# Kernel tuning notes

Hardware: AMD Instinct MI355X
Metric: run time of the kernel (lower is better)

The kernel has to match this reference:

```python
import jax, jax.numpy as jnp
import numpy as np

K = 20  # hard-coded k in both DynamicEdgeConv layers


def knn_idx(x, k):
    # pairwise squared distances: |xi|^2 + |xj|^2 - 2 xi.xj  -> [N, N]
    sq = jnp.sum(x * x, axis=-1)
    d = sq[:, None] + sq[None, :] - 2.0 * (x @ x.T)
    _, idx = jax.lax.top_k(-d, k)  # k nearest (self included at dist 0)
    return idx  # [N, k]


def edge_conv(x, idx, W, b):
    # message = MLP([x_i, x_j - x_i]), aggregate = max over neighbors
    xi = x[:, None, :]                       # [N, 1, d]
    xj = x[idx]                              # [N, k, d] gather
    e = jnp.concatenate([jnp.broadcast_to(xi, xj.shape), xj - xi], axis=-1)  # [N, k, 2d]
    h = jax.nn.relu(e @ W + b)               # [N, k, out]
    return jnp.max(h, axis=1)                # [N, out]


def setup_inputs() -> dict:
    key = jax.random.key(0)
    ks = jax.random.split(key, 9)
    N, num_classes = 16384, 40
    s = lambda fan_in: 1.0 / np.sqrt(fan_in)
    return {
        "x": jax.random.normal(ks[0], (N, 3), dtype=jnp.float32),
        "W1": jax.random.normal(ks[1], (6, 64), dtype=jnp.float32) * s(6),
        "b1": jax.random.normal(ks[2], (64,), dtype=jnp.float32) * s(6),
        "W2": jax.random.normal(ks[3], (128, 128), dtype=jnp.float32) * s(128),
        "b2": jax.random.normal(ks[4], (128,), dtype=jnp.float32) * s(128),
        "fc1_w": jax.random.normal(ks[5], (128, 128), dtype=jnp.float32) * s(128),
        "fc1_b": jax.random.normal(ks[6], (128,), dtype=jnp.float32) * s(128),
        "fc2_w": jax.random.normal(ks[7], (128, num_classes), dtype=jnp.float32) * s(128),
        "fc2_b": jax.random.normal(ks[8], (num_classes,), dtype=jnp.float32) * s(128),
    }


def reference(x, W1, b1, W2, b2, fc1_w, fc1_b, fc2_w, fc2_b):
    h = edge_conv(x, knn_idx(x, K), W1, b1)   # [N, 64], kNN on xyz
    h = edge_conv(h, knn_idx(h, K), W2, b2)   # [N, 128], kNN rebuilt on features
    h = jax.nn.relu(h @ fc1_w + fc1_b)
    return h @ fc2_w + fc2_b                  # [N, num_classes]
```

## Files before the change

kernel.cpp:

```cpp
#include <hip/hip_runtime.h>
#include <math.h>

#define N_PTS 16384
#define KNN 20
#define NRANGE 4
#define C_RANGE (N_PTS / NRANGE)
#define QCAPW 256
#define QSW 257
#define HQS 65

#define HBIN_SHIFT 22
#define HBIN_BASE 222

__device__ __forceinline__ unsigned short f2bf(float f) {
  unsigned int u = __float_as_uint(f);
  unsigned int r = (u + 0x7fffu + ((u >> 16) & 1u)) >> 16;
  return (unsigned short)r;
}
__device__ __forceinline__ float bf2f(unsigned short b) {
  return __uint_as_float(((unsigned int)b) << 16);
}

__global__ void pack_kernel(const float* __restrict__ x, float4* __restrict__ xp,
                            unsigned short* __restrict__ xpa,
                            unsigned short* __restrict__ xpb) {
  int i = blockIdx.x*256 + threadIdx.x;
  float v0 = x[i*3+0], v1 = x[i*3+1], v2 = x[i*3+2];
  {
    #pragma clang fp contract(off)
    xp[i] = make_float4(v0, v1, v2, v0*v0 + v1*v1 + v2*v2);
  }
  unsigned int h0 = f2bf(v0), h1 = f2bf(v1), h2 = f2bf(v2);
  unsigned int l0 = f2bf(v0 - bf2f((unsigned short)h0));
  unsigned int l1 = f2bf(v1 - bf2f((unsigned short)h1));
  unsigned int l2 = f2bf(v2 - bf2f((unsigned short)h2));
  unsigned int ua0 = h0 | (h1<<16), ua1 = h2 | (l0<<16), ua2 = l1 | (l2<<16);
  unsigned int ub0 = h0 | (h1<<16), ub1 = h2 | (h0<<16), ub2 = h1 | (h2<<16);
  unsigned int ub3 = l0 | (l1<<16), ub4 = l2 | (l0<<16), ub5 = l1 | (l2<<16);
  uint4* pa = (uint4*)(xpa + (size_t)i*32);
  uint4* pb = (uint4*)(xpb + (size_t)i*32);
  uint4 z; z.x = 0u; z.y = 0u; z.z = 0u; z.w = 0u;
  uint4 A0; A0.x = ua0; A0.y = ua1; A0.z = ua2; A0.w = ua0;
  uint4 A1; A1.x = ua1; A1.y = ua2; A1.z = 0u;  A1.w = 0u;
  uint4 B0; B0.x = ub0; B0.y = ub1; B0.z = ub2; B0.w = ub3;
  uint4 B1; B1.x = ub4; B1.y = ub5; B1.z = 0u;  B1.w = 0u;
  pa[0] = A0; pa[1] = A1; pa[2] = z; pa[3] = z;
  pb[0] = B0; pb[1] = B1; pb[2] = z; pb[3] = z;
}

__global__ void sq64_kernel(const float* __restrict__ h, float* __restrict__ sq) {
  int i = blockIdx.x * blockDim.x + threadIdx.x;
  const float4* r = (const float4*)(h + (long)i*64);
  {
    #pragma clang fp contract(off)
    float ax=0.f, ay=0.f, az=0.f, aw=0.f;
    for (int t=0; t<16; t++) {
      float4 v = r[t];
      ax += v.x*v.x; ay += v.y*v.y; az += v.z*v.z; aw += v.w*v.w;
    }
    sq[i] = (ax+ay)+(az+aw);
  }
}

__global__ void tobf16_kernel(const float* __restrict__ h,
                              unsigned short* __restrict__ bh) {
  int g = blockIdx.x*256 + threadIdx.x;
  float4 v = ((const float4*)h)[g];
  ushort4 hv;
  hv.x = f2bf(v.x); hv.y = f2bf(v.y); hv.z = f2bf(v.z); hv.w = f2bf(v.w);
  ((ushort4*)bh)[g] = hv;
}

__global__ __launch_bounds__(256, 2) void seed64_kernel(const float* __restrict__ h,
                                                        const float* __restrict__ sq,
                                                        const int* __restrict__ idx1,
                                                        float* __restrict__ wsd) {
  int i = blockIdx.x*256 + threadIdx.x;
  float4 q4[16];
  const float4* qrow = (const float4*)(h + (size_t)i*64);
  #pragma unroll
  for (int t=0;t<16;t++) q4[t] = qrow[t];
  float sqi = sq[i];
  float wmax = 0.f;
  for (int k=0;k<KNN;k++) {
    int j = idx1[i*KNN+k];
    const float4* crow = (const float4*)(h + (size_t)j*64);
    float acc = 0.f;
    #pragma unroll 4
    for (int t=0;t<16;t++) {
      float4 c = crow[t];
      acc += q4[t].x*c.x; acc += q4[t].y*c.y; acc += q4[t].z*c.z; acc += q4[t].w*c.w;
    }
    float sqj = sq[j];
    float d = (sqi + sqj) - 2.0f*acc;
    d += (sqi + sqj)*3e-5f + 1e-25f;
    wmax = fmaxf(wmax, d);
  }
  wsd[i] = wmax;
}

__device__ __forceinline__ void t20_replace_rescan(float (&rd)[KNN], int (&ri)[KNN],
                                                   float &maxd, int &maxi, int &maxp,
                                                   float e, int ei) {
  #pragma unroll
  for (int k = 0; k < KNN; k++) if (k == maxp) { rd[k] = e; ri[k] = ei; }
  float md = rd[0]; int mi = ri[0]; int mp = 0;
  #pragma unroll
  for (int k = 1; k < KNN; k++) {
    bool g = (rd[k] > md) || (rd[k] == md && ri[k] > mi);
    md = g ? rd[k] : md; mi = g ? ri[k] : mi; mp = g ? k : mp;
  }
  maxd = md; maxi = mi; maxp = mp;
}

#define WAVE_LDS_FENCE() asm volatile("s_waitcnt lgkmcnt(0)" ::: "memory")

typedef __bf16 bf16x8 __attribute__((ext_vector_type(8)));
typedef float f32x4 __attribute__((ext_vector_type(4)));
#define MFMA16(A,B,C) __builtin_amdgcn_mfma_f32_16x16x32_bf16((A),(B),(C),0,0,0)
#define SCALE3 0.9998f
#define SCALE_HH 0.995f

__device__ __forceinline__ int hbin(float uu) {
  uu = fmaxf(uu, 1e-20f);
  int b = (int)(__float_as_uint(uu) >> HBIN_SHIFT) - HBIN_BASE;
  return b < 0 ? 0 : (b > 63 ? 63 : b);
}

__global__ __launch_bounds__(128, 2) void knn64_wq(const float* __restrict__ h1,
                                                   const unsigned short* __restrict__ hbh,
                                                   const float* __restrict__ sqh,
                                                   const float* __restrict__ wsd,
                                                   float* __restrict__ pd,
                                                   int* __restrict__ pi) {
  __shared__ unsigned short qq[2][32][QSW];
  __shared__ float w19[2][32];
  __shared__ int   cnt[2][32];

  int tid = threadIdx.x;
  int wv = tid >> 6;
  int l  = tid & 63;
  int qb = blockIdx.x >> 2, rg = blockIdx.x & 3;
  int q0 = qb*64, c0 = rg*C_RANGE;
  int qw0 = q0 + wv*32;

  float rd[KNN]; int ri[KNN];
  #pragma unroll
  for (int k = 0; k < KNN; k++) { rd[k] = INFINITY; ri[k] = 0x7fffffff; }
  float maxd = INFINITY; int maxi = 0x7fffffff; int maxp = 0;

  float wsv = INFINITY, sqi = 0.f;
  if (l < 32) {
    wsv = wsd[qw0 + l]; sqi = sqh[qw0 + l];
    w19[wv][l] = wsv; cnt[wv][l] = 0;
  }

  int cn   = l & 15;
  int koff = (l >> 4) * 8;

  bf16x8 a00, a01, a10, a11;
  {
    size_t ar = (size_t)(qw0 + cn) * 64 + koff;
    a00 = *(const bf16x8*)(hbh + ar);
    a01 = *(const bf16x8*)(hbh + ar + 32);
    size_t br = (size_t)(qw0 + 16 + cn) * 64 + koff;
    a10 = *(const bf16x8*)(hbh + br);
    a11 = *(const bf16x8*)(hbh + br + 32);
  }

  float qsl[8], wq[8];
  #pragma unroll
  for (int v = 0; v < 8; v++)
    qsl[v] = sqh[qw0 + (v>>2)*16 + (l>>4)*4 + (v&3)] * SCALE_HH;
  WAVE_LDS_FENCE();
  #pragma unroll
  for (int v = 0; v < 8; v++) wq[v] = w19[wv][(v>>2)*16 + (l>>4)*4 + (v&3)];

  bf16x8 Bp[8], Bq[8]; float Cp[4], Cq[4];

  #define LOADC64(WIN, T0, B, C) do { int cw_ = c0 + (WIN)*256;            \
    _Pragma("unroll")                                                      \
    for (int t_ = 0; t_ < 4; t_++) {                                       \
      size_t br_ = (size_t)(cw_ + ((T0)+t_)*16 + cn) * 64 + koff;          \
      B[2*t_]   = *(const bf16x8*)(hbh + br_);                             \
      B[2*t_+1] = *(const bf16x8*)(hbh + br_ + 32);                        \
      C[t_] = sqh[cw_ + ((T0)+t_)*16 + cn];                                \
    } } while (0)

  #define TILE64(T, B0, B1, CS) do {                                       \
    f32x4 z_ = {0.f, 0.f, 0.f, 0.f};                                       \
    f32x4 d0_ = MFMA16(a00, B0, z_); d0_ = MFMA16(a01, B1, d0_);           \
    f32x4 d1_ = MFMA16(a10, B0, z_); d1_ = MFMA16(a11, B1, d1_);           \
    float csl_ = (CS) * SCALE_HH;                                          \
    _Pragma("unroll")                                                      \
    for (int v = 0; v < 8; v++) {                                          \
      float av_ = (v < 4) ? d0_[v] : d1_[v-4];                             \
      float dd_ = fmaf(-2.f, av_, qsl[v] + csl_);                          \
      if (dd_ <= wq[v]) {                                                  \
        int lq_ = (v>>2)*16 + (l>>4)*4 + (v&3);                            \
        int slot_ = atomicAdd(&cnt[wv][lq_], 1);                           \
        qq[wv][lq_][slot_] = (unsigned short)((T)*16 + cn);                \
      }                                                                    \
    } } while (0)

  #define CHUNK64(B, C, T0)                                                \
    TILE64((T0)+0, B[0], B[1], C[0]); TILE64((T0)+1, B[2], B[3], C[1]);    \
    TILE64((T0)+2, B[4], B[5], C[2]); TILE64((T0)+3, B[6], B[7], C[3])

  LOADC64(0, 0, Bp, Cp);
  for (int win = 0; win < C_RANGE/256; win++) {
    int cw0 = c0 + win*256;
    LOADC64(win, 4, Bq, Cq);
    CHUNK64(Bp, Cp, 0);
    LOADC64(win, 8, Bp, Cp);
    CHUNK64(Bq, Cq, 4);
    LOADC64(win, 12, Bq, Cq);
    CHUNK64(Bp, Cp, 8);
    if (win < C_RANGE/256 - 1) LOADC64(win+1, 0, Bp, Cp);
    CHUNK64(Bq, Cq, 12);

    WAVE_LDS_FENCE();
    int myc = (l < 32) ? cnt[wv][l] : 0;
    if (__any(myc != 0)) {
      if (myc) {
        const float4* qr = (const float4*)(h1 + (size_t)(qw0 + l)*64);
        for (int s = 0; s < myc; s++) {
          int j = cw0 + (int)qq[wv][l][s];
          const float4* cr = (const float4*)(h1 + (size_t)j*64);
          float a = 0.f;
          #pragma unroll 4
          for (int t = 0; t < 16; t++) {
            float4 q = qr[t], c = cr[t];
            a = fmaf(q.x, c.x, a); a = fmaf(q.y, c.y, a);
            a = fmaf(q.z, c.z, a); a = fmaf(q.w, c.w, a);
          }
          float e = (sqi + sqh[j]) - 2.0f*a;
          if (e < maxd || (e == maxd && j < maxi))
            t20_replace_rescan(rd, ri, maxd, maxi, maxp, e, j);
        }
        cnt[wv][l] = 0;
        w19[wv][l] = fminf(maxd, wsv);
      }
      WAVE_LDS_FENCE();
      #pragma unroll
      for (int v = 0; v < 8; v++) wq[v] = w19[wv][(v>>2)*16 + (l>>4)*4 + (v&3)];
    }
  }
  #undef LOADC64
  #undef TILE64
  #undef CHUNK64

  if (l < 32) {
    size_t o = ((size_t)(qw0 + l)*NRANGE + rg)*KNN;
    for (int k = 0; k < KNN; k++) {
      float md = rd[0]; int mi = ri[0]; int mp = 0;
      #pragma unroll
      for (int t = 1; t < KNN; t++) {
        bool g = (rd[t] < md) || (rd[t] == md && ri[t] < mi);
        md = g ? rd[t] : md; mi = g ? ri[t] : mi; mp = g ? t : mp;
      }
      pd[o+k] = md; pi[o+k] = mi;
      #pragma unroll
      for (int t = 0; t < KNN; t++) if (t == mp) rd[t] = INFINITY;
    }
  }
}

__global__ __launch_bounds__(128, 2) void knn3_wq(const float4* __restrict__ xp,
                                                  const unsigned short* __restrict__ xpa,
                                                  const unsigned short* __restrict__ xpb,
                                                  float* __restrict__ pd,
                                                  int* __restrict__ pi) {
  __shared__ unsigned short qq[2][32][QSW];
  __shared__ float w19[2][32];
  __shared__ int   cnt[2][32];

  int tid = threadIdx.x;
  int wv = tid >> 6;
  int l  = tid & 63;
  int qb = blockIdx.x >> 2, rg = blockIdx.x & 3;
  int q0 = qb*64, c0 = rg*C_RANGE;
  int qw0 = q0 + wv*32;

  float rd[KNN]; int ri[KNN];
  #pragma unroll
  for (int k = 0; k < KNN; k++) { rd[k] = INFINITY; ri[k] = 0x7fffffff; }
  float maxd = INFINITY; int maxi = 0x7fffffff; int maxp = 0;

  float4 qv4 = make_float4(0.f, 0.f, 0.f, 0.f);
  if (l < 32) {
    cnt[wv][l] = 0;
    qv4 = xp[qw0 + l];
  }

  int cn   = l & 15;
  int koff = (l >> 4) * 8;

  bf16x8 aq0 = *(const bf16x8*)(xpa + (size_t)(qw0 + cn)*32 + koff);
  bf16x8 aq1 = *(const bf16x8*)(xpa + (size_t)(qw0 + 16 + cn)*32 + koff);

  float qsr[8], qsp[8];
  #pragma unroll
  for (int v = 0; v < 8; v++) {
    qsr[v] = xp[qw0 + (v>>2)*16 + (l>>4)*4 + (v&3)].w;
    qsp[v] = qsr[v] * SCALE3;
  }

  unsigned int* hw = (unsigned int*)&qq[wv][0][0];
  for (int t = l; t < 32*HQS; t += 64) hw[t] = 0u;
  WAVE_LDS_FENCE();

  for (int win = 0; win < 16; win += 4) {
    int cw0 = c0 + win*256;
    #pragma unroll
    for (int t = 0; t < 16; t++) {
      int ct = cw0 + t*16;
      bf16x8 bb = *(const bf16x8*)(xpb + (size_t)(ct + cn)*32 + koff);
      f32x4 z = {0.f, 0.f, 0.f, 0.f};
      f32x4 d0 = MFMA16(aq0, bb, z);
      f32x4 d1 = MFMA16(aq1, bb, z);
      float csr = xp[ct + cn].w;
      #pragma unroll
      for (int v = 0; v < 8; v++) {
        float av = (v < 4) ? d0[v] : d1[v-4];
        float uu = fmaf(-2.f, av, (qsr[v] + csr) * 1.0002f);
        int lq = (v>>2)*16 + (l>>4)*4 + (v&3);
        atomicAdd(&hw[lq*HQS + hbin(uu)], 1u);
      }
    }
  }
  WAVE_LDS_FENCE();

  float wsv = INFINITY;
  if (l < 32) {
    unsigned int c = 0; int bsel = 64;
    for (int b = 0; b < 64; b++) {
      c += hw[l*HQS + b];
      if (bsel == 64 && c >= 20u) bsel = b;
    }
    if (bsel < 63)
      wsv = __uint_as_float((unsigned int)(bsel + HBIN_BASE + 1) << HBIN_SHIFT);
  }
  WAVE_LDS_FENCE();
  if (l < 32) {
    w19[wv][l] = wsv;
    cnt[wv][l] = 0;
  }
  WAVE_LDS_FENCE();
  float wq[8];
  #pragma unroll
  for (int v = 0; v < 8; v++) wq[v] = w19[wv][(v>>2)*16 + (l>>4)*4 + (v&3)];

  bf16x8 Bp[4], Bq[4]; float Cp[4], Cq[4];

  #define LOADC3(WIN, T0, B, C) do { int cw_ = c0 + (WIN)*256;             \
    _Pragma("unroll")                                                      \
    for (int t_ = 0; t_ < 4; t_++) {                                       \
      int ct_ = cw_ + ((T0)+t_)*16;                                        \
      B[t_] = *(const bf16x8*)(xpb + (size_t)(ct_ + cn)*32 + koff);        \
      C[t_] = xp[ct_ + cn].w;                                              \
    } } while (0)

  #define TILE3(T, BB, CS) do {                                            \
    f32x4 z_ = {0.f, 0.f, 0.f, 0.f};                                       \
    f32x4 d0_ = MFMA16(aq0, BB, z_);                                       \
    f32x4 d1_ = MFMA16(aq1, BB, z_);                                       \
    float csp_ = (CS) * SCALE3;                                            \
    _Pragma("unroll")                                                      \
    for (int v = 0; v < 8; v++) {                                          \
      float av_ = (v < 4) ? d0_[v] : d1_[v-4];                             \
      float dd_ = fmaf(-2.f, av_, qsp[v] + csp_);                          \
      if (dd_ <= wq[v]) {                                                  \
        int lq_ = (v>>2)*16 + (l>>4)*4 + (v&3);                            \
        int slot_ = atomicAdd(&cnt[wv][lq_], 1);                           \
        qq[wv][lq_][slot_] = (unsigned short)((T)*16 + cn);                \
      }                                                                    \
    } } while (0)

  #define CHUNK3(B, C, T0)                                                 \
    TILE3((T0)+0, B[0], C[0]); TILE3((T0)+1, B[1], C[1]);                  \
    TILE3((T0)+2, B[2], C[2]); TILE3((T0)+3, B[3], C[3])

  LOADC3(0, 0, Bp, Cp);
  for (int win = 0; win < 16; win++) {
    int cw0 = c0 + win*256;
    LOADC3(win, 4, Bq, Cq);
    CHUNK3(Bp, Cp, 0);
    LOADC3(win, 8, Bp, Cp);
    CHUNK3(Bq, Cq, 4);
    LOADC3(win, 12, Bq, Cq);
    CHUNK3(Bp, Cp, 8);
    if (win < 15) LOADC3(win+1, 0, Bp, Cp);
    CHUNK3(Bq, Cq, 12);

    WAVE_LDS_FENCE();
    int myc = (l < 32) ? cnt[wv][l] : 0;
    if (__any(myc != 0)) {
      if (myc) {
        for (int s = 0; s < myc; s++) {
          int j = cw0 + (int)qq[wv][l][s];
          float4 cv4 = xp[j];
          float e = (qv4.w + cv4.w)
                  - 2.0f*(qv4.x*cv4.x + qv4.y*cv4.y + qv4.z*cv4.z);
          if (e < maxd || (e == maxd && j < maxi))
            t20_replace_rescan(rd, ri, maxd, maxi, maxp, e, j);
        }
        cnt[wv][l] = 0;
        w19[wv][l] = fminf(maxd, wsv);
      }
      WAVE_LDS_FENCE();
      #pragma unroll
      for (int v = 0; v < 8; v++) wq[v] = w19[wv][(v>>2)*16 + (l>>4)*4 + (v&3)];
    }
  }
  #undef LOADC3
  #undef TILE3
  #undef CHUNK3

  if (l < 32) {
    size_t o = ((size_t)(qw0 + l)*NRANGE + rg)*KNN;
    for (int k = 0; k < KNN; k++) {
      float md = rd[0]; int mi = ri[0]; int mp = 0;
      #pragma unroll
      for (int t = 1; t < KNN; t++) {
        bool g = (rd[t] < md) || (rd[t] == md && ri[t] < mi);
        md = g ? rd[t] : md; mi = g ? ri[t] : mi; mp = g ? t : mp;
      }
      pd[o+k] = md; pi[o+k] = mi;
      #pragma unroll
      for (int t = 0; t < KNN; t++) if (t == mp) rd[t] = INFINITY;
    }
  }
}

__global__ void knn_merge_kernel(const float* __restrict__ pd, const int* __restrict__ pi,
                                 int* __restrict__ out_idx) {
  int qi = blockIdx.x*256 + threadIdx.x;
  const float* bd = pd + (size_t)qi*NRANGE*KNN;
  const int*   bi = pi + (size_t)qi*NRANGE*KNN;
  int ptr[NRANGE];
  #pragma unroll
  for (int r=0;r<NRANGE;r++) ptr[r] = 0;
  for (int k = 0; k < KNN; k++) {
    float best = INFINITY; int besti = 0x7fffffff; int br = 0;
    #pragma unroll
    for (int r = 0; r < NRANGE; r++) {
      float d = bd[r*KNN + ptr[r]];
      int   ii = bi[r*KNN + ptr[r]];
      bool better = (ptr[r] < KNN) && (d < best || (d == best && ii < besti));
      if (better) { best = d; besti = ii; br = r; }
    }
    #pragma unroll
    for (int r=0;r<NRANGE;r++) ptr[r] += (r == br) ? 1 : 0;
    out_idx[qi*KNN + k] = besti;
  }
}

__global__ void cg1_kernel(const float* __restrict__ x, const float* __restrict__ W1,
                           const float* __restrict__ b1,
                           float* __restrict__ C1, float* __restrict__ G1) {
  int gid = blockIdx.x*256 + threadIdx.x;
  int i = gid >> 6, c = gid & 63;
  float x0 = x[i*3+0], x1 = x[i*3+1], x2 = x[i*3+2];
  float wt0 = W1[0*64+c], wt1 = W1[1*64+c], wt2 = W1[2*64+c];
  float wb0 = W1[3*64+c], wb1 = W1[4*64+c], wb2 = W1[5*64+c];
  C1[gid] = x0*(wt0-wb0) + x1*(wt1-wb1) + x2*(wt2-wb2) + b1[c];
  G1[gid] = x0*wb0 + x1*wb1 + x2*wb2;
}

template<int C>
__global__ void maxrelu4_kernel(const float* __restrict__ Ci, const float* __restrict__ G,
                                const int* __restrict__ idx, float* __restrict__ out) {
  int gid = blockIdx.x*256 + threadIdx.x;
  int i = gid / (C/4), c4 = gid % (C/4);
  float4 base = *(const float4*)(Ci + (size_t)i*C + c4*4);
  float4 m = make_float4(-INFINITY, -INFINITY, -INFINITY, -INFINITY);
  for (int j=0; j<KNN; j++) {
    int jj = idx[i*KNN + j];
    float4 g = *(const float4*)(G + (size_t)jj*C + c4*4);
    m.x = fmaxf(m.x, base.x + g.x); m.y = fmaxf(m.y, base.y + g.y);
    m.z = fmaxf(m.z, base.z + g.z); m.w = fmaxf(m.w, base.w + g.w);
  }
  float4 o;
  o.x = fmaxf(m.x, 0.0f); o.y = fmaxf(m.y, 0.0f);
  o.z = fmaxf(m.z, 0.0f); o.w = fmaxf(m.w, 0.0f);
  *(float4*)(out + (size_t)i*C + c4*4) = o;
}

__global__ void cg2_kernel(const float* __restrict__ h1, const float* __restrict__ W2,
                           const float* __restrict__ b2,
                           float* __restrict__ C2, float* __restrict__ G2) {
  int gid = blockIdx.x*256 + threadIdx.x;
  int i = gid >> 7, c = gid & 127;
  float a = 0.f, g = 0.f;
  for (int d=0; d<64; d++) {
    float hv = h1[i*64 + d];
    float wt = W2[d*128 + c];
    float wb = W2[(d+64)*128 + c];
    a += hv * (wt - wb);
    g += hv * wb;
  }
  C2[gid] = a + b2[c];
  G2[gid] = g;
}

__global__ void fc1_kernel(const float* __restrict__ h2, const float* __restrict__ w,
                           const float* __restrict__ b, float* __restrict__ out) {
  int gid = blockIdx.x*256 + threadIdx.x;
  int i = gid >> 7, c = gid & 127;
  float a = 0.f;
  for (int d=0; d<128; d++) a += h2[i*128+d] * w[d*128+c];
  out[gid] = fmaxf(a + b[c], 0.0f);
}

__global__ void fc2_kernel(const float* __restrict__ f1, const float* __restrict__ w,
                           const float* __restrict__ b, float* __restrict__ out) {
  int gid = blockIdx.x*256 + threadIdx.x;
  int i = gid / 40, c = gid - i*40;
  float a = 0.f;
  for (int d=0; d<128; d++) a += f1[i*128+d] * w[d*40+c];
  out[gid] = a + b[c];
}

extern "C" void kernel_launch(void* const* d_in, const int* in_sizes, int n_in,
                              void* d_out, int out_size, void* d_ws, size_t ws_size,
                              hipStream_t stream) {
  (void)in_sizes; (void)n_in; (void)out_size; (void)ws_size;
  const float* x     = (const float*)d_in[0];
  const float* W1    = (const float*)d_in[1];
  const float* b1    = (const float*)d_in[2];
  const float* W2    = (const float*)d_in[3];
  const float* b2    = (const float*)d_in[4];
  const float* fc1_w = (const float*)d_in[5];
  const float* fc1_b = (const float*)d_in[6];
  const float* fc2_w = (const float*)d_in[7];
  const float* fc2_b = (const float*)d_in[8];
  float* out = (float*)d_out;

  char* ws = (char*)d_ws;
  float4* xp4 = (float4*)(ws + 0);
  float*  sqh = (float*) (ws + 262144);
  int*    idx = (int*)   (ws + 327680);
  float*  h1  = (float*) (ws + 1671168);
  unsigned short* xpa = (unsigned short*)(ws + 1671168);
  unsigned short* xpb = (unsigned short*)(ws + 2719744);
  unsigned short* hbh = (unsigned short*)(ws + 5865472);
  float*  wsd = (float*) (ws + 10059776);
  float*  h2  = (float*) (ws + 5865472);
  float*  A   = (float*) (ws + 14254080);
  float*  C1  = A;
  float*  G1  = (float*) (ws + 14254080 + 4194304);
  float*  C2  = A;
  float*  f1  = A;
  float*  G2  = (float*) (ws + 22642688);
  int*    pi  = (int*)   (ws + 14254080);
  float*  pd  = (float*) (ws + 22642688);

  pack_kernel  <<<64,   256, 0, stream>>>(x, xp4, xpa, xpb);
  knn3_wq      <<<1024, 128, 0, stream>>>(xp4, xpa, xpb, pd, pi);
  knn_merge_kernel<<<64,256, 0, stream>>>(pd, pi, idx);
  cg1_kernel   <<<4096, 256, 0, stream>>>(x, W1, b1, C1, G1);
  maxrelu4_kernel<64> <<<1024, 256, 0, stream>>>(C1, G1, idx, h1);
  tobf16_kernel<<<1024, 256, 0, stream>>>(h1, hbh);
  sq64_kernel  <<<64,   256, 0, stream>>>(h1, sqh);
  seed64_kernel<<<64,   256, 0, stream>>>(h1, sqh, idx, wsd);
  knn64_wq     <<<1024, 128, 0, stream>>>(h1, hbh, sqh, wsd, pd, pi);
  knn_merge_kernel<<<64,256, 0, stream>>>(pd, pi, idx);
  cg2_kernel   <<<8192, 256, 0, stream>>>(h1, W2, b2, C2, G2);
  maxrelu4_kernel<128><<<2048, 256, 0, stream>>>(C2, G2, idx, h2);
  fc1_kernel   <<<8192, 256, 0, stream>>>(h2, fc1_w, fc1_b, f1);
  fc2_kernel   <<<2560, 256, 0, stream>>>(f1, fc2_w, fc2_b, out);
}
```

Measured before the change: 1.078 ms.

## Fuse bf16 conversion into maxrelu, fuse maxrelu+fc1+fc2, split seed kernel

The bf16 conversion is folded into the first max-relu aggregation kernel. The second aggregation, fc1 and fc2 become one per-point block that keeps h2 and f1 in shared memory. The seed kernel splits each point's 20 neighbours across 4 lanes and reduces them with shuffles, giving 4x more threads. Together these remove kernel launches and global round-trips for h2 and f1. The cost is that the fused MLP block is small (128 threads per point), so weight reuse depends on cache.

```diff
diff --git a/kernel.cpp b/kernel.cpp
--- a/kernel.cpp
+++ b/kernel.cpp
@@ -62,27 +62,19 @@
   }
 }
 
-__global__ void tobf16_kernel(const float* __restrict__ h,
-                              unsigned short* __restrict__ bh) {
-  int g = blockIdx.x*256 + threadIdx.x;
-  float4 v = ((const float4*)h)[g];
-  ushort4 hv;
-  hv.x = f2bf(v.x); hv.y = f2bf(v.y); hv.z = f2bf(v.z); hv.w = f2bf(v.w);
-  ((ushort4*)bh)[g] = hv;
-}
-
 __global__ __launch_bounds__(256, 2) void seed64_kernel(const float* __restrict__ h,
                                                         const float* __restrict__ sq,
                                                         const int* __restrict__ idx1,
                                                         float* __restrict__ wsd) {
-  int i = blockIdx.x*256 + threadIdx.x;
+  int gid = blockIdx.x*256 + threadIdx.x;
+  int i = gid >> 2, part = gid & 3;
   float4 q4[16];
   const float4* qrow = (const float4*)(h + (size_t)i*64);
   #pragma unroll
   for (int t=0;t<16;t++) q4[t] = qrow[t];
   float sqi = sq[i];
   float wmax = 0.f;
-  for (int k=0;k<KNN;k++) {
+  for (int k=part*5;k<part*5+5;k++) {
     int j = idx1[i*KNN+k];
     const float4* crow = (const float4*)(h + (size_t)j*64);
     float acc = 0.f;
@@ -96,7 +88,9 @@
     d += (sqi + sqj)*3e-5f + 1e-25f;
     wmax = fmaxf(wmax, d);
   }
-  wsd[i] = wmax;
+  wmax = fmaxf(wmax, __shfl_xor(wmax, 1));
+  wmax = fmaxf(wmax, __shfl_xor(wmax, 2));
+  if (part == 0) wsd[i] = wmax;
 }
 
 __device__ __forceinline__ void t20_replace_rescan(float (&rd)[KNN], int (&ri)[KNN],
@@ -468,23 +462,26 @@
   G1[gid] = x0*wb0 + x1*wb1 + x2*wb2;
 }
 
-template<int C>
-__global__ void maxrelu4_kernel(const float* __restrict__ Ci, const float* __restrict__ G,
-                                const int* __restrict__ idx, float* __restrict__ out) {
+__global__ void mrt64_kernel(const float* __restrict__ Ci, const float* __restrict__ G,
+                             const int* __restrict__ idx, float* __restrict__ out,
+                             unsigned short* __restrict__ bh) {
   int gid = blockIdx.x*256 + threadIdx.x;
-  int i = gid / (C/4), c4 = gid % (C/4);
-  float4 base = *(const float4*)(Ci + (size_t)i*C + c4*4);
+  int i = gid >> 4, c4 = gid & 15;
+  float4 base = *(const float4*)(Ci + (size_t)i*64 + c4*4);
   float4 m = make_float4(-INFINITY, -INFINITY, -INFINITY, -INFINITY);
   for (int j=0; j<KNN; j++) {
     int jj = idx[i*KNN + j];
-    float4 g = *(const float4*)(G + (size_t)jj*C + c4*4);
+    float4 g = *(const float4*)(G + (size_t)jj*64 + c4*4);
     m.x = fmaxf(m.x, base.x + g.x); m.y = fmaxf(m.y, base.y + g.y);
     m.z = fmaxf(m.z, base.z + g.z); m.w = fmaxf(m.w, base.w + g.w);
   }
   float4 o;
   o.x = fmaxf(m.x, 0.0f); o.y = fmaxf(m.y, 0.0f);
   o.z = fmaxf(m.z, 0.0f); o.w = fmaxf(m.w, 0.0f);
-  *(float4*)(out + (size_t)i*C + c4*4) = o;
+  *(float4*)(out + (size_t)i*64 + c4*4) = o;
+  ushort4 hv;
+  hv.x = f2bf(o.x); hv.y = f2bf(o.y); hv.z = f2bf(o.z); hv.w = f2bf(o.w);
+  ((ushort4*)bh)[i*16 + c4] = hv;
 }
 
 __global__ void cg2_kernel(const float* __restrict__ h1, const float* __restrict__ W2,
@@ -504,22 +501,34 @@
   G2[gid] = g;
 }
 
-__global__ void fc1_kernel(const float* __restrict__ h2, const float* __restrict__ w,
-                           const float* __restrict__ b, float* __restrict__ out) {
-  int gid = blockIdx.x*256 + threadIdx.x;
-  int i = gid >> 7, c = gid & 127;
+__global__ __launch_bounds__(128) void mrfc_kernel(const float* __restrict__ C2,
+                                                   const float* __restrict__ G2,
+                                                   const int* __restrict__ idx,
+                                                   const float* __restrict__ w1,
+                                                   const float* __restrict__ b1,
+                                                   const float* __restrict__ w2,
+                                                   const float* __restrict__ b2,
+                                                   float* __restrict__ out) {
+  __shared__ float h2r[128];
+  __shared__ float f1r[128];
+  int i = blockIdx.x, c = threadIdx.x;
+  float base = C2[(size_t)i*128 + c];
+  float m = -INFINITY;
+  for (int j = 0; j < KNN; j++) {
+    int jj = idx[i*KNN + j];
+    m = fmaxf(m, base + G2[(size_t)jj*128 + c]);
+  }
+  h2r[c] = fmaxf(m, 0.0f);
+  __syncthreads();
   float a = 0.f;
-  for (int d=0; d<128; d++) a += h2[i*128+d] * w[d*128+c];
-  out[gid] = fmaxf(a + b[c], 0.0f);
-}
-
-__global__ void fc2_kernel(const float* __restrict__ f1, const float* __restrict__ w,
-                           const float* __restrict__ b, float* __restrict__ out) {
-  int gid = blockIdx.x*256 + threadIdx.x;
-  int i = gid / 40, c = gid - i*40;
-  float a = 0.f;
-  for (int d=0; d<128; d++) a += f1[i*128+d] * w[d*40+c];
-  out[gid] = a + b[c];
+  for (int d = 0; d < 128; d++) a += h2r[d] * w1[d*128 + c];
+  f1r[c] = fmaxf(a + b1[c], 0.0f);
+  __syncthreads();
+  if (c < 40) {
+    float a2 = 0.f;
+    for (int d = 0; d < 128; d++) a2 += f1r[d] * w2[d*40 + c];
+    out[i*40 + c] = a2 + b2[c];
+  }
 }
 
 extern "C" void kernel_launch(void* const* d_in, const int* in_sizes, int n_in,
@@ -546,28 +555,23 @@
   unsigned short* xpb = (unsigned short*)(ws + 2719744);
   unsigned short* hbh = (unsigned short*)(ws + 5865472);
   float*  wsd = (float*) (ws + 10059776);
-  float*  h2  = (float*) (ws + 5865472);
   float*  A   = (float*) (ws + 14254080);
   float*  C1  = A;
   float*  G1  = (float*) (ws + 14254080 + 4194304);
   float*  C2  = A;
-  float*  f1  = A;
   float*  G2  = (float*) (ws + 22642688);
   int*    pi  = (int*)   (ws + 14254080);
   float*  pd  = (float*) (ws + 22642688);
 
-  pack_kernel  <<<64,   256, 0, stream>>>(x, xp4, xpa, xpb);
-  knn3_wq      <<<1024, 128, 0, stream>>>(xp4, xpa, xpb, pd, pi);
-  knn_merge_kernel<<<64,256, 0, stream>>>(pd, pi, idx);
-  cg1_kernel   <<<4096, 256, 0, stream>>>(x, W1, b1, C1, G1);
-  maxrelu4_kernel<64> <<<1024, 256, 0, stream>>>(C1, G1, idx, h1);
-  tobf16_kernel<<<1024, 256, 0, stream>>>(h1, hbh);
-  sq64_kernel  <<<64,   256, 0, stream>>>(h1, sqh);
-  seed64_kernel<<<64,   256, 0, stream>>>(h1, sqh, idx, wsd);
-  knn64_wq     <<<1024, 128, 0, stream>>>(h1, hbh, sqh, wsd, pd, pi);
-  knn_merge_kernel<<<64,256, 0, stream>>>(pd, pi, idx);
-  cg2_kernel   <<<8192, 256, 0, stream>>>(h1, W2, b2, C2, G2);
-  maxrelu4_kernel<128><<<2048, 256, 0, stream>>>(C2, G2, idx, h2);
-  fc1_kernel   <<<8192, 256, 0, stream>>>(h2, fc1_w, fc1_b, f1);
-  fc2_kernel   <<<2560, 256, 0, stream>>>(f1, fc2_w, fc2_b, out);
-}
+  pack_kernel  <<<64,    256, 0, stream>>>(x, xp4, xpa, xpb);
+  knn3_wq      <<<1024,  128, 0, stream>>>(xp4, xpa, xpb, pd, pi);
+  knn_merge_kernel<<<64, 256, 0, stream>>>(pd, pi, idx);
+  cg1_kernel   <<<4096,  256, 0, stream>>>(x, W1, b1, C1, G1);
+  mrt64_kernel <<<1024,  256, 0, stream>>>(C1, G1, idx, h1, hbh);
+  sq64_kernel  <<<64,    256, 0, stream>>>(h1, sqh);
+  seed64_kernel<<<256,   256, 0, stream>>>(h1, sqh, idx, wsd);
+  knn64_wq     <<<1024,  128, 0, stream>>>(h1, hbh, sqh, wsd, pd, pi);
+  knn_merge_kernel<<<64, 256, 0, stream>>>(pd, pi, idx);
+  cg2_kernel   <<<8192,  256, 0, stream>>>(h1, W2, b2, C2, G2);
+  mrfc_kernel  <<<16384, 128, 0, stream>>>(C2, G2, idx, fc1_w, fc1_b, fc2_w, fc2_b, out);
+}
```

New measurement: 968.9 us. -10.1%, faster.
